# Performance work log

Measured on AMD Instinct MI355X. Metric: run time of the kernel, lower is better.

Reference implementation:

```python
import jax, jax.numpy as jnp
import numpy as np
import math

B, L = 16, 4096
N = B * L            # total nodes; node 0 is the (masked) root
E = N - 1            # one parent edge per non-root node
D_IN, D_OUT, HEADS = 512, 256, 4
SLOPE = 0.2          # PyG GATConv default negative_slope
PRUNE_FRAC = 0.3


def gelu(x):
    return 0.5 * x * (1.0 + jnp.tanh(math.sqrt(2.0 / math.pi) * (x + 0.044715 * x ** 3)))


def remove_nodes_func(parent, remove):
    # parent[i] = parent node id of node i+1; remove[j] = 1 iff node j+1 removed.
    for _ in range(5):
        aug_rem = jnp.concatenate([jnp.zeros(1, jnp.int32), remove])
        aug_par = jnp.concatenate([jnp.zeros(1, jnp.int32), parent])
        pr = aug_rem[parent]                               # is my parent removed?
        parent = pr * aug_par[parent] + (1 - pr) * parent  # grandparent if so
    return parent


def remove_nodes_and_edges(edge_index, map_index):
    src, par = edge_index[0], edge_index[1]
    rem = jnp.zeros(N, jnp.int32).at[map_index].set(1)     # removal flag per node id (>=1)
    edge_mask = 1 - rem[src]                               # drop edges whose child node removed
    emr = rem[1:]                                          # == zeros(E).at[map_index-1].set(1)
    temp = remove_nodes_func(par, emr)
    ei_new = jnp.stack([src, temp]) * edge_mask[None, :]   # removed edges collapse to (0,0)
    node_mask_upd = jnp.concatenate([jnp.ones(1, jnp.float32), 1.0 - emr.astype(jnp.float32)])
    return ei_new, node_mask_upd


def gat_conv(xin, edge_index, gat_w, att_src, att_dst, gat_b):
    # PyG GATConv: concat=True, add_self_loops=True, eval mode (attention dropout off)
    h = (xin @ gat_w).reshape(N, HEADS, D_OUT)
    loop = jnp.arange(N, dtype=edge_index.dtype)
    src = jnp.concatenate([edge_index[0], loop])
    dst = jnp.concatenate([edge_index[1], loop])
    a_src = jnp.einsum('nhc,hc->nh', h, att_src)
    a_dst = jnp.einsum('nhc,hc->nh', h, att_dst)
    alpha = jax.nn.leaky_relu(a_src[src] + a_dst[dst], SLOPE)       # [Etot, H]
    m = jax.ops.segment_max(alpha, dst, num_segments=N)
    e = jnp.exp(alpha - m[dst])
    s = jax.ops.segment_sum(e, dst, num_segments=N)
    coef = e / (s[dst] + 1e-16)
    out = jax.ops.segment_sum(coef[:, :, None] * h[src], dst, num_segments=N)
    return out.reshape(N, HEADS * D_OUT) + gat_b


def setup_inputs():
    key = jax.random.key(0)
    ks = jax.random.split(key, 10)
    x = jax.random.normal(ks[0], (N, D_IN), jnp.float32)
    statement_rep = jax.random.normal(ks[1], (N, D_IN), jnp.float32)
    node_mask = (jax.random.uniform(ks[2], (B, L)) > 0.3).astype(jnp.float32)
    node_mask = node_mask.at[0, 0].set(0.0)  # root node never scored/pruned
    type_id = jax.random.randint(ks[3], (B, L), 0, 2, dtype=jnp.int32)
    child = jnp.arange(1, N, dtype=jnp.int32)
    parent = jnp.floor(jax.random.uniform(ks[4], (E,)) * child).astype(jnp.int32)  # parent < child
    edge_index = jnp.stack([child, parent])
    edge_index_ent = edge_index
    s = 0.02
    scorer_w = jax.random.normal(ks[5], (2 * D_IN, 1), jnp.float32) * s
    scorer_b = jnp.zeros((1,), jnp.float32)
    emb_w = jax.random.normal(ks[6], (2, D_OUT), jnp.float32) * s
    emb_b = jnp.zeros((D_OUT,), jnp.float32)
    gat_w = jax.random.normal(ks[7], (2 * D_IN + D_OUT, HEADS * D_OUT), jnp.float32) * s
    att_src = jax.random.normal(ks[8], (HEADS, D_OUT), jnp.float32) * s
    att_dst = jax.random.normal(ks[9], (HEADS, D_OUT), jnp.float32) * s
    gat_b = jnp.zeros((HEADS * D_OUT,), jnp.float32)
    return {"x": x, "edge_index": edge_index, "edge_index_ent": edge_index_ent,
            "statement_rep": statement_rep, "node_mask": node_mask, "type_id": type_id,
            "scorer_w": scorer_w, "scorer_b": scorer_b, "emb_w": emb_w, "emb_b": emb_b,
            "gat_w": gat_w, "att_src": att_src, "att_dst": att_dst, "gat_b": gat_b}


def reference(x, edge_index, edge_index_ent, statement_rep, node_mask, type_id,
              scorer_w, scorer_b, emb_w, emb_b, gat_w, att_src, att_dst, gat_b):
    del edge_index_ent  # threaded through the original but never used
    nm = node_mask.reshape(-1)
    tid = type_id.reshape(-1)
    one_hot = jax.nn.one_hot(tid, 2, dtype=jnp.float32)
    type_emb = gelu(one_hot @ emb_w + emb_b)
    # --- single GNN layer (num_layers=1), with top-k node pruning ---
    node_score = (jnp.concatenate([x, statement_rep], 1) @ scorer_w + scorer_b)[:, 0] * nm
    nnz = int(jnp.count_nonzero(node_score))  # eager; k is data-dependent in the original
    if int(nnz * PRUNE_FRAC) != 0:
        k = int(nnz * PRUNE_FRAC + 1)
        masked = jnp.where(node_score != 0, node_score, jnp.inf)
        _, map_index = jax.lax.top_k(-masked, k)  # k smallest nonzero scores -> node ids
        edge_index, upd = remove_nodes_and_edges(edge_index, map_index)
        nm = nm * upd
    xin = jnp.concatenate([x, statement_rep, type_emb], 1)
    out = gelu(gat_conv(xin, edge_index, gat_w, att_src, att_dst, gat_b))
    # feature dropout runs in eval as identity here (deterministic reference)
    return out, nm.reshape(B, L)
```

## Files before the change

### kernel.cpp

```cpp
#include <hip/hip_runtime.h>
#include <cstdint>
#include <cstddef>

#define N_NODES 65536
#define E_EDGES 65535
#define DIN     512
#define KDIM    1024
#define JDIM    1024
#define HEADS   4
#define DOUT    256

typedef short   short8  __attribute__((ext_vector_type(8)));
typedef float   floatx4 __attribute__((ext_vector_type(4)));

__device__ inline float bf2f(unsigned short u){
  union { unsigned int i; float f; } c; c.i = ((unsigned int)u) << 16; return c.f;
}
__device__ inline unsigned short f2bf(float f){
  union { float f; unsigned int i; } c; c.f = f;
  unsigned int r = c.i + 0x7FFFu + ((c.i >> 16) & 1u);
  return (unsigned short)(r >> 16);
}
__device__ inline unsigned int okey(float f){
  union { float f; unsigned int u; } c; c.f = f;
  return (c.u & 0x80000000u) ? ~c.u : (c.u | 0x80000000u);
}
__device__ inline float unokey(unsigned int k){
  union { unsigned int u; float f; } c;
  c.u = (k & 0x80000000u) ? (k ^ 0x80000000u) : ~k;
  return c.f;
}
__device__ inline float leaky(float x){ return x >= 0.f ? x : 0.2f * x; }
__device__ inline float gelu_f(float x){
  return 0.5f * x * (1.f + tanhf(0.7978845608028654f * (x + 0.044715f * x * x * x)));
}

__global__ void k_prep(const float* __restrict__ x, const float* __restrict__ sr,
                       const float* __restrict__ nmask, const float* __restrict__ sw,
                       const float* __restrict__ sb, unsigned short* __restrict__ xs,
                       float* __restrict__ score){
  int i = blockIdx.x, t = threadIdx.x;
  float4 v;
  if (t < 128) v = *(const float4*)(x  + (size_t)i*DIN + 4*t);
  else         v = *(const float4*)(sr + (size_t)i*DIN + 4*(t-128));
  const float4 w = *(const float4*)(sw + 4*t);
  double part = (double)v.x*(double)w.x + (double)v.y*(double)w.y
              + (double)v.z*(double)w.z + (double)v.w*(double)w.w;
  ushort4 o; o.x = f2bf(v.x); o.y = f2bf(v.y); o.z = f2bf(v.z); o.w = f2bf(v.w);
  *(ushort4*)(xs + (size_t)i*KDIM + 4*t) = o;
  for (int sdel = 32; sdel; sdel >>= 1) part += __shfl_down(part, sdel);
  __shared__ double red[4];
  if ((t & 63) == 0) red[t >> 6] = part;
  __syncthreads();
  if (t == 0){
    double s = red[0] + red[1] + red[2] + red[3] + (double)sb[0];
    score[i] = (float)s * nmask[i];
  }
}

__global__ void k_nnz(const float* __restrict__ score, int* scal){
  int i = blockIdx.x*256 + threadIdx.x;
  int nz = (score[i] != 0.f) ? 1 : 0;
  unsigned long long b = __ballot(nz);
  if ((threadIdx.x & 63) == 0) atomicAdd(&scal[0], (int)__popcll(b));
}

__global__ void k_makekey(const float* __restrict__ score, unsigned int* __restrict__ key){
  int i = blockIdx.x*256 + threadIdx.x;
  float v = score[i];
  if (v == 0.f) v = __builtin_inff();
  key[i] = okey(v);
}

__global__ void k_initsel(int* scal){
  int nnz = scal[0];
  double prod = (double)nnz * 0.3;
  scal[1] = ((int)prod != 0) ? 1 : 0;
  int k = (int)(prod + 1.0);
  scal[2] = k; scal[3] = 0; scal[4] = k;
}

__global__ void k_hist(const unsigned int* __restrict__ key, unsigned int* __restrict__ hist,
                       const int* __restrict__ scal, int pass){
  __shared__ unsigned int lh[256];
  int t = threadIdx.x;
  lh[t] = 0; __syncthreads();
  int i = blockIdx.x*256 + t;
  unsigned int kv = key[i];
  unsigned int pref = (unsigned int)scal[3];
  bool ok = (pass == 0) || ((kv >> (32 - 8*pass)) == pref);
  if (ok) atomicAdd(&lh[(kv >> (24 - 8*pass)) & 255u], 1u);
  __syncthreads();
  if (lh[t]) atomicAdd(&hist[t], lh[t]);
}

__global__ void k_select(unsigned int* __restrict__ hist, int* __restrict__ scal){
  __shared__ unsigned int h[256];
  int t = threadIdx.x;
  h[t] = hist[t];
  __syncthreads();
  if (t == 0){
    unsigned int r = (unsigned int)scal[4];
    unsigned int cum = 0, pref = (unsigned int)scal[3];
    for (int b = 0; b < 256; b++){
      unsigned int c = h[b];
      if (cum + c >= r){
        scal[3] = (int)((pref << 8) | (unsigned int)b);
        scal[4] = (int)(r - cum);
        break;
      }
      cum += c;
    }
  }
  __syncthreads();
  hist[t] = 0;
}

__global__ void k_mark(const unsigned int* __restrict__ key, int* __restrict__ scal,
                       int* __restrict__ rem, int* __restrict__ eqlist){
  if (!scal[1]) return;
  int i = blockIdx.x*256 + threadIdx.x;
  unsigned int Ks = (unsigned int)scal[3];
  unsigned int kv = key[i];
  if (kv < Ks) rem[i] = 1;
  else if (kv == Ks){
    int p = atomicAdd(&scal[5], 1);
    if (p < 4096) eqlist[p] = i;
  }
}

__global__ void k_ties(int* __restrict__ scal, int* __restrict__ eqlist, int* __restrict__ rem){
  if (!scal[1]) return;
  int m = scal[5]; if (m > 4096) m = 4096;
  int need = scal[4]; if (need > m) need = m;
  for (int it = 0; it < need; it++){
    int best = 0x7FFFFFFF, bj = -1;
    for (int j = 0; j < m; j++){ int v = eqlist[j]; if (v < best){ best = v; bj = j; } }
    if (bj < 0) break;
    rem[best] = 1; eqlist[bj] = 0x7FFFFFFF;
  }
}

__global__ void k_remap(const int* __restrict__ pin, const int* __restrict__ rem,
                        int* __restrict__ pout){
  int e = blockIdx.x*256 + threadIdx.x;
  if (e >= E_EDGES) return;
  int p = pin[e];
  pout[e] = rem[p] ? (p == 0 ? 0 : pin[p-1]) : p;
}

__global__ void k_edges(const int* __restrict__ srcIn, const int* __restrict__ pfin,
                        const int* __restrict__ rem, int* __restrict__ srcF,
                        int* __restrict__ dstF, int* __restrict__ cnt){
  int e = blockIdx.x*256 + threadIdx.x;
  if (e >= E_EDGES) return;
  int s = srcIn[e];
  if (rem[s]){ srcF[e] = 0; dstF[e] = -1; }
  else {
    srcF[e] = s;
    int d = pfin[e];
    dstF[e] = d;
    atomicAdd(&cnt[d], 1);
  }
}

__global__ void k_scan1(const int* __restrict__ cnt, int* __restrict__ offs,
                        int* __restrict__ bsum){
  int b = blockIdx.x, t = threadIdx.x, i = b*256 + t;
  int v = cnt[i];
  int lane = t & 63, wv = t >> 6;
  int xv = v;
  for (int o2 = 1; o2 < 64; o2 <<= 1){ int y = __shfl_up(xv, o2); if (lane >= o2) xv += y; }
  __shared__ int wt_[4];
  if (lane == 63) wt_[wv] = xv;
  __syncthreads();
  int add = 0;
  for (int k2 = 0; k2 < wv; k2++) add += wt_[k2];
  offs[i] = xv + add - v;
  if (t == 255) bsum[b] = xv + add;
}

__global__ void k_scan2(int* __restrict__ bsum){
  int t = threadIdx.x;
  int v = bsum[t];
  int lane = t & 63, wv = t >> 6;
  int xv = v;
  for (int o2 = 1; o2 < 64; o2 <<= 1){ int y = __shfl_up(xv, o2); if (lane >= o2) xv += y; }
  __shared__ int wt_[4];
  if (lane == 63) wt_[wv] = xv;
  __syncthreads();
  int add = 0;
  for (int k2 = 0; k2 < wv; k2++) add += wt_[k2];
  bsum[t] = xv + add - v;
}

__global__ void k_scan3(int* __restrict__ offs, const int* __restrict__ bsum,
                        int* __restrict__ cur){
  int b = blockIdx.x, t = threadIdx.x, i = b*256 + t;
  int v = offs[i] + bsum[b];
  offs[i] = v; cur[i] = v;
}

__global__ void k_fill(const int* __restrict__ dstF, int* __restrict__ cur,
                       int* __restrict__ elist){
  int e = blockIdx.x*256 + threadIdx.x;
  if (e >= E_EDGES) return;
  int d = dstF[e]; if (d < 0) return;
  int pos = atomicAdd(&cur[d], 1);
  elist[pos] = e;
}

__global__ void k_wt(const float* __restrict__ gw, unsigned short* __restrict__ wtb){
  __shared__ float tile[32][33];
  int kt = blockIdx.x*32, jt = blockIdx.y*32;
  int tx = threadIdx.x, ty = threadIdx.y;
  for (int r = ty; r < 32; r += 8) tile[r][tx] = gw[(size_t)(kt+r)*JDIM + jt + tx];
  __syncthreads();
  for (int r = ty; r < 32; r += 8) wtb[(size_t)(jt+r)*KDIM + kt + tx] = f2bf(tile[tx][r]);
}

__global__ void k_tc(const float* __restrict__ embw, const float* __restrict__ embb,
                     const float* __restrict__ gw, float* __restrict__ tc){
  int g = blockIdx.x*256 + threadIdx.x;
  int te = g >> 10, j = g & 1023;
  float acc = 0.f;
  for (int c = 0; c < DOUT; c++){
    float e = gelu_f(embw[te*DOUT + c] + embb[c]);
    acc += e * gw[(size_t)(KDIM + c)*JDIM + j];
  }
  tc[te*JDIM + j] = acc;
}

#define BKG 64
__global__ __launch_bounds__(512, 2) void k_gemm(const unsigned short* __restrict__ xs,
    const unsigned short* __restrict__ wtb, const float* __restrict__ tc,
    const int* __restrict__ tid, unsigned short* __restrict__ hmat){
  __shared__ unsigned short As[2][256*BKG];
  __shared__ unsigned short Bs[2][256*BKG];
  int bid = blockIdx.x;
  int xcd = bid & 7, tq = bid >> 3;
  int jb = tq & 3, ip = (tq >> 2)*8 + xcd;
  int rowbase = ip*256, colbase = jb*256;
  int t = threadIdx.x, wave = t >> 6, lane = t & 63;
  int wm = (wave >> 2)*128, wn = (wave & 3)*64;
  floatx4 acc[8][4];
  floatx4 zero = {0.f, 0.f, 0.f, 0.f};
  #pragma unroll
  for (int a = 0; a < 8; a++)
    #pragma unroll
    for (int b = 0; b < 4; b++) acc[a][b] = zero;

  int srow = lane >> 3;
  int scol = (lane & 7)*8;

  auto STAGE = [&](int buf, int kt){
    int k0 = kt*BKG;
    #pragma unroll
    for (int r = 0; r < 4; r++){
      int ci = r*8 + wave;
      int row = ci*8 + srow;
      const unsigned short* ga = xs  + (size_t)(rowbase + row)*KDIM + k0 + scol;
      __builtin_amdgcn_global_load_lds((const __attribute__((address_space(1))) void*)ga,
          (__attribute__((address_space(3))) void*)(&As[buf][ci*512 + lane*8]), 16, 0, 0);
      const unsigned short* gb = wtb + (size_t)(colbase + row)*KDIM + k0 + scol;
      __builtin_amdgcn_global_load_lds((const __attribute__((address_space(1))) void*)gb,
          (__attribute__((address_space(3))) void*)(&Bs[buf][ci*512 + lane*8]), 16, 0, 0);
    }
  };

  int rr = lane & 15, rq = (lane >> 4)*8;
  auto COMPUTE = [&](int buf){
    #pragma unroll
    for (int ks = 0; ks < 2; ks++){
      short8 af[8], bfr[4];
      #pragma unroll
      for (int mi = 0; mi < 8; mi++)
        af[mi]  = *(const short8*)(&As[buf][(wm + mi*16 + rr)*BKG + ks*32 + rq]);
      #pragma unroll
      for (int ni = 0; ni < 4; ni++)
        bfr[ni] = *(const short8*)(&Bs[buf][(wn + ni*16 + rr)*BKG + ks*32 + rq]);
      #pragma unroll
      for (int mi = 0; mi < 8; mi++)
        #pragma unroll
        for (int ni = 0; ni < 4; ni++)
          acc[mi][ni] = __builtin_amdgcn_mfma_f32_16x16x32_bf16(af[mi], bfr[ni], acc[mi][ni], 0, 0, 0);
    }
  };

  const int NT = KDIM / BKG;
  STAGE(0, 0);
  __syncthreads();
  int cur = 0;
  for (int kt = 0; kt < NT - 1; kt++){
    STAGE(cur ^ 1, kt + 1);
    COMPUTE(cur);
    __syncthreads();
    cur ^= 1;
  }
  COMPUTE(cur);

  int q = lane >> 4, cc = lane & 15;
  #pragma unroll
  for (int mi = 0; mi < 8; mi++){
    #pragma unroll
    for (int reg = 0; reg < 4; reg++){
      int rowg = rowbase + wm + mi*16 + q*4 + reg;
      int tt = tid[rowg];
      #pragma unroll
      for (int ni = 0; ni < 4; ni++){
        int col = colbase + wn + ni*16 + cc;
        float v = acc[mi][ni][reg] + tc[tt*JDIM + col];
        hmat[(size_t)rowg*JDIM + col] = f2bf(v);
      }
    }
  }
}

__global__ void k_att(const unsigned short* __restrict__ hmat, const float* __restrict__ atts,
                      const float* __restrict__ attd, float* __restrict__ asrc,
                      float* __restrict__ adst){
  int i = blockIdx.x, t = threadIdx.x;
  int hd = t >> 6, c = (t & 63)*4;
  ushort4 hv = *(const ushort4*)(hmat + (size_t)i*JDIM + hd*DOUT + c);
  float h0 = bf2f(hv.x), h1 = bf2f(hv.y), h2 = bf2f(hv.z), h3 = bf2f(hv.w);
  float4 ws_ = *(const float4*)(atts + hd*DOUT + c);
  float4 wd_ = *(const float4*)(attd + hd*DOUT + c);
  float ps = h0*ws_.x + h1*ws_.y + h2*ws_.z + h3*ws_.w;
  float pd = h0*wd_.x + h1*wd_.y + h2*wd_.z + h3*wd_.w;
  for (int sdel = 32; sdel; sdel >>= 1){ ps += __shfl_down(ps, sdel); pd += __shfl_down(pd, sdel); }
  if ((t & 63) == 0){ asrc[i*HEADS + hd] = ps; adst[i*HEADS + hd] = pd; }
}

__global__ void k_max(const int* __restrict__ srcF, const int* __restrict__ dstF,
                      const float* __restrict__ asrc, const float* __restrict__ adst,
                      unsigned int* __restrict__ mkey){
  int idx = blockIdx.x*256 + threadIdx.x;
  if (idx >= E_EDGES + N_NODES) return;
  int s, d;
  if (idx < E_EDGES){ d = dstF[idx]; if (d < 0) return; s = srcF[idx]; }
  else { s = d = idx - E_EDGES; }
  for (int hd = 0; hd < HEADS; hd++){
    float al = leaky(asrc[s*HEADS + hd] + adst[d*HEADS + hd]);
    atomicMax(&mkey[d*HEADS + hd], okey(al));
  }
}

__global__ void k_sum(const int* __restrict__ srcF, const int* __restrict__ dstF,
                      const float* __restrict__ asrc, const float* __restrict__ adst,
                      const unsigned int* __restrict__ mkey, float* __restrict__ ssum,
                      const int* __restrict__ scal){
  int idx = blockIdx.x*256 + threadIdx.x;
  if (idx >= E_EDGES + N_NODES) return;
  int s, d; float wgt = 1.f;
  if (idx < E_EDGES){ d = dstF[idx]; if (d < 0) return; s = srcF[idx]; }
  else {
    s = d = idx - E_EDGES;
    if (d == 0 && scal[1]) wgt = 1.f + (float)scal[2];
  }
  for (int hd = 0; hd < HEADS; hd++){
    float al = leaky(asrc[s*HEADS + hd] + adst[d*HEADS + hd]);
    float e = expf(al - unokey(mkey[d*HEADS + hd]));
    atomicAdd(&ssum[d*HEADS + hd], wgt * e);
  }
}

__global__ void k_agg(const unsigned short* __restrict__ hmat, const int* __restrict__ srcF,
                      const float* __restrict__ asrc, const float* __restrict__ adst,
                      const unsigned int* __restrict__ mkey, const float* __restrict__ ssum,
                      const int* __restrict__ offs, const int* __restrict__ cnt,
                      const int* __restrict__ elist, const float* __restrict__ gatb,
                      const int* __restrict__ scal, float* __restrict__ out){
  int n = blockIdx.x, t = threadIdx.x;
  int hd = t >> 6;
  float mh = unokey(mkey[n*HEADS + hd]);
  float sh = ssum[n*HEADS + hd] + 1e-16f;
  float adn = adst[n*HEADS + hd];
  float a0 = 0.f, a1 = 0.f, a2 = 0.f, a3 = 0.f;
  {
    float al = leaky(asrc[n*HEADS + hd] + adn);
    float coef = expf(al - mh) / sh;
    if (n == 0 && scal[1]) coef *= (1.f + (float)scal[2]);
    ushort4 hv = *(const ushort4*)(hmat + (size_t)n*JDIM + 4*t);
    a0 += coef*bf2f(hv.x); a1 += coef*bf2f(hv.y); a2 += coef*bf2f(hv.z); a3 += coef*bf2f(hv.w);
  }
  int o0 = offs[n], c_ = cnt[n];
  for (int q2 = 0; q2 < c_; q2++){
    int e = elist[o0 + q2];
    int s = srcF[e];
    float al = leaky(asrc[s*HEADS + hd] + adn);
    float coef = expf(al - mh) / sh;
    ushort4 hv = *(const ushort4*)(hmat + (size_t)s*JDIM + 4*t);
    a0 += coef*bf2f(hv.x); a1 += coef*bf2f(hv.y); a2 += coef*bf2f(hv.z); a3 += coef*bf2f(hv.w);
  }
  const float4 gb = *(const float4*)(gatb + 4*t);
  float4 ov;
  ov.x = gelu_f(a0 + gb.x); ov.y = gelu_f(a1 + gb.y);
  ov.z = gelu_f(a2 + gb.z); ov.w = gelu_f(a3 + gb.w);
  *(float4*)(out + (size_t)n*JDIM + 4*t) = ov;
}

__global__ void k_nm(const float* __restrict__ nmask, const int* __restrict__ rem,
                     float* __restrict__ nmout){
  int i = blockIdx.x*256 + threadIdx.x;
  float u = (i == 0) ? 1.f : (1.f - (float)rem[i]);
  nmout[i] = nmask[i] * u;
}

extern "C" void kernel_launch(void* const* d_in, const int* in_sizes, int n_in,
                              void* d_out, int out_size, void* d_ws, size_t ws_size,
                              hipStream_t stream){
  (void)in_sizes; (void)n_in; (void)out_size; (void)ws_size;
  const float* x    = (const float*)d_in[0];
  const int*  eidx  = (const int*)d_in[1];
  const float* sr   = (const float*)d_in[3];
  const float* nmask= (const float*)d_in[4];
  const int*  tid   = (const int*)d_in[5];
  const float* sw   = (const float*)d_in[6];
  const float* sb   = (const float*)d_in[7];
  const float* embw = (const float*)d_in[8];
  const float* embb = (const float*)d_in[9];
  const float* gw   = (const float*)d_in[10];
  const float* atts = (const float*)d_in[11];
  const float* attd = (const float*)d_in[12];
  const float* gatb = (const float*)d_in[13];
  float* out = (float*)d_out;

  char* w = (char*)d_ws;
  size_t o = 0;
  auto alloc = [&](size_t bytes){ size_t r = o; o += (bytes + 255) & ~(size_t)255; return r; };
  size_t o_cnt  = alloc((size_t)N_NODES*4);
  size_t o_mkey = alloc((size_t)N_NODES*HEADS*4);
  size_t o_ssum = alloc((size_t)N_NODES*HEADS*4);
  size_t o_rem  = alloc((size_t)N_NODES*4);
  size_t o_hist = alloc(256*4);
  size_t o_scal = alloc(64);
  size_t o_eq   = alloc(4096*4);
  size_t zero_bytes = o;
  size_t o_score= alloc((size_t)N_NODES*4);
  size_t o_key  = alloc((size_t)N_NODES*4);
  size_t o_pA   = alloc((size_t)E_EDGES*4);
  size_t o_pB   = alloc((size_t)E_EDGES*4);
  size_t o_srcF = alloc((size_t)E_EDGES*4);
  size_t o_dstF = alloc((size_t)E_EDGES*4);
  size_t o_off  = alloc((size_t)N_NODES*4);
  size_t o_cur  = alloc((size_t)N_NODES*4);
  size_t o_el   = alloc((size_t)E_EDGES*4);
  size_t o_bsum = alloc(256*4);
  size_t o_asrc = alloc((size_t)N_NODES*HEADS*4);
  size_t o_adst = alloc((size_t)N_NODES*HEADS*4);
  size_t o_tc   = alloc((size_t)2*JDIM*4);
  size_t o_wt   = alloc((size_t)JDIM*KDIM*2);
  size_t o_xs   = alloc((size_t)N_NODES*KDIM*2);
  size_t o_h    = alloc((size_t)N_NODES*JDIM*2);

  int* cnt   = (int*)(w + o_cnt);
  unsigned int* mkey = (unsigned int*)(w + o_mkey);
  float* ssum = (float*)(w + o_ssum);
  int* rem   = (int*)(w + o_rem);
  unsigned int* hist = (unsigned int*)(w + o_hist);
  int* scal  = (int*)(w + o_scal);
  int* eqlist= (int*)(w + o_eq);
  float* score = (float*)(w + o_score);
  unsigned int* key = (unsigned int*)(w + o_key);
  int* pA = (int*)(w + o_pA);
  int* pB = (int*)(w + o_pB);
  int* srcF = (int*)(w + o_srcF);
  int* dstF = (int*)(w + o_dstF);
  int* offs = (int*)(w + o_off);
  int* cur  = (int*)(w + o_cur);
  int* elist= (int*)(w + o_el);
  int* bsum = (int*)(w + o_bsum);
  float* asrc = (float*)(w + o_asrc);
  float* adst = (float*)(w + o_adst);
  float* tc = (float*)(w + o_tc);
  unsigned short* wtb = (unsigned short*)(w + o_wt);
  unsigned short* xs  = (unsigned short*)(w + o_xs);
  unsigned short* hmat= (unsigned short*)(w + o_h);

  hipMemsetAsync(w, 0, zero_bytes, stream);

  k_prep<<<N_NODES, 256, 0, stream>>>(x, sr, nmask, sw, sb, xs, score);
  k_nnz<<<N_NODES/256, 256, 0, stream>>>(score, scal);
  k_makekey<<<N_NODES/256, 256, 0, stream>>>(score, key);
  k_initsel<<<1, 1, 0, stream>>>(scal);
  for (int p = 0; p < 4; p++){
    k_hist<<<N_NODES/256, 256, 0, stream>>>(key, hist, scal, p);
    k_select<<<1, 256, 0, stream>>>(hist, scal);
  }
  k_mark<<<N_NODES/256, 256, 0, stream>>>(key, scal, rem, eqlist);
  k_ties<<<1, 1, 0, stream>>>(scal, eqlist, rem);

  const int* par_in = eidx + E_EDGES;
  int egrid = (E_EDGES + 255)/256;
  k_remap<<<egrid, 256, 0, stream>>>(par_in, rem, pA);
  k_remap<<<egrid, 256, 0, stream>>>(pA, rem, pB);
  k_remap<<<egrid, 256, 0, stream>>>(pB, rem, pA);
  k_remap<<<egrid, 256, 0, stream>>>(pA, rem, pB);
  k_remap<<<egrid, 256, 0, stream>>>(pB, rem, pA);

  k_edges<<<egrid, 256, 0, stream>>>(eidx, pA, rem, srcF, dstF, cnt);
  k_scan1<<<256, 256, 0, stream>>>(cnt, offs, bsum);
  k_scan2<<<1, 256, 0, stream>>>(bsum);
  k_scan3<<<256, 256, 0, stream>>>(offs, bsum, cur);
  k_fill<<<egrid, 256, 0, stream>>>(dstF, cur, elist);

  k_wt<<<dim3(32,32), dim3(32,8), 0, stream>>>(gw, wtb);
  k_tc<<<8, 256, 0, stream>>>(embw, embb, gw, tc);
  k_gemm<<<1024, 512, 0, stream>>>(xs, wtb, tc, tid, hmat);
  k_att<<<N_NODES, 256, 0, stream>>>(hmat, atts, attd, asrc, adst);

  int mg = (E_EDGES + N_NODES + 255)/256;
  k_max<<<mg, 256, 0, stream>>>(srcF, dstF, asrc, adst, mkey);
  k_sum<<<mg, 256, 0, stream>>>(srcF, dstF, asrc, adst, mkey, ssum, scal);
  k_agg<<<N_NODES, 256, 0, stream>>>(hmat, srcF, asrc, adst, mkey, ssum, offs, cnt,
                                     elist, gatb, scal, out);
  k_nm<<<N_NODES/256, 256, 0, stream>>>(nmask, rem, out + (size_t)N_NODES*JDIM);
}
```

Before: 1.067 ms.

## Fuse attention-logit dots into GEMM epilogue and merge key building into prep

The per-head attention dot products (a_src, a_dst) are now computed in the GEMM epilogue from fp32 accumulators. They are reduced across lanes with shuffles and across waves through shared memory, which removes the separate k_att pass that re-read the whole bf16 hidden matrix. k_prep now handles one row per wave, writes 8-wide vectors and emits the ordered selection key directly, so k_makekey is gone. k_tc precomputes the GELU type embeddings once in shared memory instead of per thread. The logits now come from unrounded fp32 values rather than bf16-rounded ones, which slightly changes numerics, and the epilogue adds register and shared-memory pressure.

Result: faster. 976.9 us (-8.5%).

```diff
diff --git a/kernel.cpp b/kernel.cpp
--- a/kernel.cpp
+++ b/kernel.cpp
@@ -11,6 +11,7 @@
 #define DOUT    256
 
 typedef short   short8  __attribute__((ext_vector_type(8)));
+typedef unsigned short ushort8 __attribute__((ext_vector_type(8)));
 typedef float   floatx4 __attribute__((ext_vector_type(4)));
 
 __device__ inline float bf2f(unsigned short u){
@@ -38,23 +39,41 @@
 __global__ void k_prep(const float* __restrict__ x, const float* __restrict__ sr,
                        const float* __restrict__ nmask, const float* __restrict__ sw,
                        const float* __restrict__ sb, unsigned short* __restrict__ xs,
-                       float* __restrict__ score){
-  int i = blockIdx.x, t = threadIdx.x;
-  float4 v;
-  if (t < 128) v = *(const float4*)(x  + (size_t)i*DIN + 4*t);
-  else         v = *(const float4*)(sr + (size_t)i*DIN + 4*(t-128));
-  const float4 w = *(const float4*)(sw + 4*t);
-  double part = (double)v.x*(double)w.x + (double)v.y*(double)w.y
-              + (double)v.z*(double)w.z + (double)v.w*(double)w.w;
-  ushort4 o; o.x = f2bf(v.x); o.y = f2bf(v.y); o.z = f2bf(v.z); o.w = f2bf(v.w);
-  *(ushort4*)(xs + (size_t)i*KDIM + 4*t) = o;
+                       float* __restrict__ score, unsigned int* __restrict__ key){
+  int lane = threadIdx.x & 63, wv = threadIdx.x >> 6;
+  int i = blockIdx.x*4 + wv;
+  const float* xr  = x  + (size_t)i*DIN + 8*lane;
+  const float* srr = sr + (size_t)i*DIN + 8*lane;
+  float4 a0 = *(const float4*)(xr);
+  float4 a1 = *(const float4*)(xr + 4);
+  float4 b0 = *(const float4*)(srr);
+  float4 b1 = *(const float4*)(srr + 4);
+  float4 w0 = *(const float4*)(sw + 8*lane);
+  float4 w1 = *(const float4*)(sw + 8*lane + 4);
+  float4 w2 = *(const float4*)(sw + 512 + 8*lane);
+  float4 w3 = *(const float4*)(sw + 512 + 8*lane + 4);
+  double part = (double)a0.x*(double)w0.x + (double)a0.y*(double)w0.y
+              + (double)a0.z*(double)w0.z + (double)a0.w*(double)w0.w
+              + (double)a1.x*(double)w1.x + (double)a1.y*(double)w1.y
+              + (double)a1.z*(double)w1.z + (double)a1.w*(double)w1.w
+              + (double)b0.x*(double)w2.x + (double)b0.y*(double)w2.y
+              + (double)b0.z*(double)w2.z + (double)b0.w*(double)w2.w
+              + (double)b1.x*(double)w3.x + (double)b1.y*(double)w3.y
+              + (double)b1.z*(double)w3.z + (double)b1.w*(double)w3.w;
+  ushort8 oa, ob;
+  oa[0]=f2bf(a0.x); oa[1]=f2bf(a0.y); oa[2]=f2bf(a0.z); oa[3]=f2bf(a0.w);
+  oa[4]=f2bf(a1.x); oa[5]=f2bf(a1.y); oa[6]=f2bf(a1.z); oa[7]=f2bf(a1.w);
+  ob[0]=f2bf(b0.x); ob[1]=f2bf(b0.y); ob[2]=f2bf(b0.z); ob[3]=f2bf(b0.w);
+  ob[4]=f2bf(b1.x); ob[5]=f2bf(b1.y); ob[6]=f2bf(b1.z); ob[7]=f2bf(b1.w);
+  *(ushort8*)(xs + (size_t)i*KDIM + 8*lane)       = oa;
+  *(ushort8*)(xs + (size_t)i*KDIM + 512 + 8*lane) = ob;
   for (int sdel = 32; sdel; sdel >>= 1) part += __shfl_down(part, sdel);
-  __shared__ double red[4];
-  if ((t & 63) == 0) red[t >> 6] = part;
-  __syncthreads();
-  if (t == 0){
-    double s = red[0] + red[1] + red[2] + red[3] + (double)sb[0];
-    score[i] = (float)s * nmask[i];
+  if (lane == 0){
+    float fs = (float)(part + (double)sb[0]);
+    float s  = fs * nmask[i];
+    score[i] = s;
+    float v = (s == 0.f) ? __builtin_inff() : s;
+    key[i] = okey(v);
   }
 }
 
@@ -63,13 +82,6 @@
   int nz = (score[i] != 0.f) ? 1 : 0;
   unsigned long long b = __ballot(nz);
   if ((threadIdx.x & 63) == 0) atomicAdd(&scal[0], (int)__popcll(b));
-}
-
-__global__ void k_makekey(const float* __restrict__ score, unsigned int* __restrict__ key){
-  int i = blockIdx.x*256 + threadIdx.x;
-  float v = score[i];
-  if (v == 0.f) v = __builtin_inff();
-  key[i] = okey(v);
 }
 
 __global__ void k_initsel(int* scal){
@@ -221,12 +233,17 @@
 
 __global__ void k_tc(const float* __restrict__ embw, const float* __restrict__ embb,
                      const float* __restrict__ gw, float* __restrict__ tc){
-  int g = blockIdx.x*256 + threadIdx.x;
+  __shared__ float eg[2][DOUT];
+  int t = threadIdx.x;
+  eg[0][t] = gelu_f(embw[t] + embb[t]);
+  eg[1][t] = gelu_f(embw[DOUT + t] + embb[t]);
+  __syncthreads();
+  int g = blockIdx.x*256 + t;
   int te = g >> 10, j = g & 1023;
   float acc = 0.f;
+  #pragma unroll 8
   for (int c = 0; c < DOUT; c++){
-    float e = gelu_f(embw[te*DOUT + c] + embb[c]);
-    acc += e * gw[(size_t)(KDIM + c)*JDIM + j];
+    acc += eg[te][c] * gw[(size_t)(KDIM + c)*JDIM + j];
   }
   tc[te*JDIM + j] = acc;
 }
@@ -234,7 +251,9 @@
 #define BKG 64
 __global__ __launch_bounds__(512, 2) void k_gemm(const unsigned short* __restrict__ xs,
     const unsigned short* __restrict__ wtb, const float* __restrict__ tc,
-    const int* __restrict__ tid, unsigned short* __restrict__ hmat){
+    const int* __restrict__ tid, const float* __restrict__ atts,
+    const float* __restrict__ attd, unsigned short* __restrict__ hmat,
+    float* __restrict__ asrc, float* __restrict__ adst){
   __shared__ unsigned short As[2][256*BKG];
   __shared__ unsigned short Bs[2][256*BKG];
   int bid = blockIdx.x;
@@ -300,35 +319,48 @@
   COMPUTE(cur);
 
   int q = lane >> 4, cc = lane & 15;
+  float att_s[4], att_d[4];
+  #pragma unroll
+  for (int ni = 0; ni < 4; ni++){
+    int cih = wn + ni*16 + cc;
+    att_s[ni] = atts[jb*DOUT + cih];
+    att_d[ni] = attd[jb*DOUT + cih];
+  }
+  __syncthreads();
+  float* sp = (float*)&As[0][0];
   #pragma unroll
   for (int mi = 0; mi < 8; mi++){
     #pragma unroll
     for (int reg = 0; reg < 4; reg++){
-      int rowg = rowbase + wm + mi*16 + q*4 + reg;
+      int rloc = wm + mi*16 + q*4 + reg;
+      int rowg = rowbase + rloc;
       int tt = tid[rowg];
+      float ps = 0.f, pd = 0.f;
       #pragma unroll
       for (int ni = 0; ni < 4; ni++){
         int col = colbase + wn + ni*16 + cc;
         float v = acc[mi][ni][reg] + tc[tt*JDIM + col];
         hmat[(size_t)rowg*JDIM + col] = f2bf(v);
+        ps += v * att_s[ni]; pd += v * att_d[ni];
+      }
+      #pragma unroll
+      for (int m2 = 1; m2 < 16; m2 <<= 1){
+        ps += __shfl_xor(ps, m2); pd += __shfl_xor(pd, m2);
+      }
+      if (cc == 0){
+        sp[(rloc*4 + (wave & 3))*2 + 0] = ps;
+        sp[(rloc*4 + (wave & 3))*2 + 1] = pd;
       }
     }
   }
-}
-
-__global__ void k_att(const unsigned short* __restrict__ hmat, const float* __restrict__ atts,
-                      const float* __restrict__ attd, float* __restrict__ asrc,
-                      float* __restrict__ adst){
-  int i = blockIdx.x, t = threadIdx.x;
-  int hd = t >> 6, c = (t & 63)*4;
-  ushort4 hv = *(const ushort4*)(hmat + (size_t)i*JDIM + hd*DOUT + c);
-  float h0 = bf2f(hv.x), h1 = bf2f(hv.y), h2 = bf2f(hv.z), h3 = bf2f(hv.w);
-  float4 ws_ = *(const float4*)(atts + hd*DOUT + c);
-  float4 wd_ = *(const float4*)(attd + hd*DOUT + c);
-  float ps = h0*ws_.x + h1*ws_.y + h2*ws_.z + h3*ws_.w;
-  float pd = h0*wd_.x + h1*wd_.y + h2*wd_.z + h3*wd_.w;
-  for (int sdel = 32; sdel; sdel >>= 1){ ps += __shfl_down(ps, sdel); pd += __shfl_down(pd, sdel); }
-  if ((t & 63) == 0){ asrc[i*HEADS + hd] = ps; adst[i*HEADS + hd] = pd; }
+  __syncthreads();
+  if (t < 256){
+    float s = 0.f, d2 = 0.f;
+    #pragma unroll
+    for (int w4 = 0; w4 < 4; w4++){ s += sp[(t*4 + w4)*2]; d2 += sp[(t*4 + w4)*2 + 1]; }
+    asrc[(size_t)(rowbase + t)*HEADS + jb] = s;
+    adst[(size_t)(rowbase + t)*HEADS + jb] = d2;
+  }
 }
 
 __global__ void k_max(const int* __restrict__ srcF, const int* __restrict__ dstF,
@@ -479,9 +511,8 @@
 
   hipMemsetAsync(w, 0, zero_bytes, stream);
 
-  k_prep<<<N_NODES, 256, 0, stream>>>(x, sr, nmask, sw, sb, xs, score);
+  k_prep<<<N_NODES/4, 256, 0, stream>>>(x, sr, nmask, sw, sb, xs, score, key);
   k_nnz<<<N_NODES/256, 256, 0, stream>>>(score, scal);
-  k_makekey<<<N_NODES/256, 256, 0, stream>>>(score, key);
   k_initsel<<<1, 1, 0, stream>>>(scal);
   for (int p = 0; p < 4; p++){
     k_hist<<<N_NODES/256, 256, 0, stream>>>(key, hist, scal, p);
@@ -506,8 +537,7 @@
 
   k_wt<<<dim3(32,32), dim3(32,8), 0, stream>>>(gw, wtb);
   k_tc<<<8, 256, 0, stream>>>(embw, embb, gw, tc);
-  k_gemm<<<1024, 512, 0, stream>>>(xs, wtb, tc, tid, hmat);
-  k_att<<<N_NODES, 256, 0, stream>>>(hmat, atts, attd, asrc, adst);
+  k_gemm<<<1024, 512, 0, stream>>>(xs, wtb, tc, tid, atts, attd, hmat, asrc, adst);
 
   int mg = (E_EDGES + N_NODES + 255)/256;
   k_max<<<mg, 256, 0, stream>>>(srcF, dstF, asrc, adst, mkey);
```
